# Kernel tuning notes

Hardware: AMD Instinct MI355X
Metric: run time of the kernel (lower is better)

## Reference

```python
import jax, jax.numpy as jnp
import numpy as np

V = 32000       # word vocab size
K = 24          # max n-grams per word (n=3, word len <= 9 -> 3*len-3 <= 24)
NG = 200000     # n_gram_size (hash table size)
E = 128         # emb_size
B, S = 16, 2048 # batch, seq_len


def setup_inputs() -> dict:
    key = jax.random.key(0)
    k1, k2, k3, k4 = jax.random.split(key, 4)
    word_idx = jax.random.randint(k1, (B, S), 0, V, dtype=jnp.int32)
    # hashed n-gram ids live in [4, NG), matching _hash(word) % (NG-4) + 4
    ngram_ids = jax.random.randint(k2, (V, K), 4, NG, dtype=jnp.int32)
    ngram_counts = jax.random.randint(k3, (V,), 1, K + 1, dtype=jnp.int32)
    # pad unused slots with id 0 (padding_idx -> zero embedding row)
    pos = jnp.arange(K)[None, :]
    ngram_ids = jnp.where(pos < ngram_counts[:, None], ngram_ids, 0)
    # special tokens (<4): direct lookup of their own embedding row, count 1
    sp = jnp.arange(4)
    ngram_ids = ngram_ids.at[sp, :].set(0).at[sp, 0].set(sp)
    ngram_counts = ngram_counts.at[sp].set(1)
    emb_table = jax.random.normal(k4, (NG, E), dtype=jnp.float32)
    return {"word_idx": word_idx, "ngram_ids": ngram_ids,
            "ngram_counts": ngram_counts, "emb_table": emb_table}


def reference(word_idx, ngram_ids, ngram_counts, emb_table):
    # nn.Embedding(padding_idx=0): row 0 is zero
    table = emb_table.at[0].set(0.0)
    g = ngram_ids[word_idx]                 # [B, S, K] gathered n-gram ids
    e = table[g]                            # [B, S, K, E] gathered embeddings
    cnt = ngram_counts[word_idx].astype(e.dtype)[..., None]  # [B, S, 1]
    # padded slots point at the zero row, so a plain sum == masked sum
    return e.sum(axis=2) / cnt              # [B, S, E] mean over n-grams
```

## Files before the change

### kernel.cpp

```cpp
#include <hip/hip_runtime.h>

#define NUM_WORDS 32768
#define KMAX 24
#define EDIM 128

__global__ __launch_bounds__(256) void ngram_emb_kernel(
    const int* __restrict__ word_idx,
    const int* __restrict__ ngram_ids,
    const int* __restrict__ ngram_counts,
    const float* __restrict__ emb_table,
    float* __restrict__ out)
{
    const int gtid = blockIdx.x * blockDim.x + threadIdx.x;
    const int word = gtid >> 6;
    const int lane = threadIdx.x & 63;
    if (word >= NUM_WORDS) return;

    const int w   = word_idx[word];
    const int cnt = ngram_counts[w];
    const int* ids = ngram_ids + (long)w * KMAX;

    int my_id = (lane < KMAX) ? ids[lane] : 0;

    float ax = 0.f, ay = 0.f;
    const long col = (long)(lane * 2);
    for (int k = 0; k < cnt; ++k) {
        const int row = __shfl(my_id, k);
        if (row != 0) {
            const float2 v = *(const float2*)(emb_table + (long)row * EDIM + col);
            ax += v.x;
            ay += v.y;
        }
    }
    const float inv = 1.0f / (float)cnt;
    float2 r; r.x = ax * inv; r.y = ay * inv;
    *(float2*)(out + (long)word * EDIM + col) = r;
}

extern "C" void kernel_launch(void* const* d_in, const int* in_sizes, int n_in,
                              void* d_out, int out_size, void* d_ws, size_t ws_size,
                              hipStream_t stream) {
    const int*   word_idx     = (const int*)d_in[0];
    const int*   ngram_ids    = (const int*)d_in[1];
    const int*   ngram_counts = (const int*)d_in[2];
    const float* emb_table    = (const float*)d_in[3];
    float*       out          = (float*)d_out;

    const int threads = 256;
    const int blocks  = (NUM_WORDS * 64) / threads;
    ngram_emb_kernel<<<blocks, threads, 0, stream>>>(
        word_idx, ngram_ids, ngram_counts, emb_table, out);
}
```

Before: 186.6 us.

## Batch embedding row loads in groups of eight with scalarized n-gram ids

The serial count-bounded loop with shuffles and a per-row branch is replaced by an unrolled loop that issues eight independent row loads at a time. The n-gram ids are loaded as wave-uniform values through readfirstlane, and a zero-id row is masked with an FMA instead of skipped. This exposes more memory-level parallelism per wave and removes the shuffle and branch overhead. In exchange it loads up to seven extra rows per word beyond the count (padding rows, mostly row 0) and uses more registers.

```diff
diff --git a/kernel.cpp b/kernel.cpp
--- a/kernel.cpp
+++ b/kernel.cpp
@@ -2,7 +2,7 @@
 
 #define NUM_WORDS 32768
 #define KMAX 24
-#define EDIM 128
+#define GROUP 8
 
 __global__ __launch_bounds__(256) void ngram_emb_kernel(
     const int* __restrict__ word_idx,
@@ -14,27 +14,41 @@
     const int gtid = blockIdx.x * blockDim.x + threadIdx.x;
     const int word = gtid >> 6;
     const int lane = threadIdx.x & 63;
-    if (word >= NUM_WORDS) return;
 
-    const int w   = word_idx[word];
+    const int w   = __builtin_amdgcn_readfirstlane(word_idx[word]);
     const int cnt = ngram_counts[w];
-    const int* ids = ngram_ids + (long)w * KMAX;
+    const int* ids = ngram_ids + w * KMAX;
 
-    int my_id = (lane < KMAX) ? ids[lane] : 0;
+    int rr[KMAX];
+#pragma unroll
+    for (int k = 0; k < KMAX; ++k)
+        rr[k] = __builtin_amdgcn_readfirstlane(ids[k]);
 
+    const float2* tbl = (const float2*)emb_table;
     float ax = 0.f, ay = 0.f;
-    const long col = (long)(lane * 2);
-    for (int k = 0; k < cnt; ++k) {
-        const int row = __shfl(my_id, k);
-        if (row != 0) {
-            const float2 v = *(const float2*)(emb_table + (long)row * EDIM + col);
-            ax += v.x;
-            ay += v.y;
+
+#pragma unroll
+    for (int g = 0; g < KMAX; g += GROUP) {
+        if (g < cnt) {
+            float2 v[GROUP];
+            float  m[GROUP];
+#pragma unroll
+            for (int j = 0; j < GROUP; ++j) {
+                const int r = rr[g + j];
+                m[j] = r ? 1.f : 0.f;
+                v[j] = tbl[(long)r * 64 + lane];
+            }
+#pragma unroll
+            for (int j = 0; j < GROUP; ++j) {
+                ax = fmaf(m[j], v[j].x, ax);
+                ay = fmaf(m[j], v[j].y, ay);
+            }
         }
     }
+
     const float inv = 1.0f / (float)cnt;
-    float2 r; r.x = ax * inv; r.y = ay * inv;
-    *(float2*)(out + (long)word * EDIM + col) = r;
+    float2 o; o.x = ax * inv; o.y = ay * inv;
+    ((float2*)out)[(long)word * 64 + lane] = o;
 }
 
 extern "C" void kernel_launch(void* const* d_in, const int* in_sizes, int n_in,
```

New measurement: 169.1 us. 9.4% less time.
